# Kernel tuning notes

Hardware: AMD Instinct MI355X
Metric: run time of the kernel (lower is better)

Reference implementation:

```python
import jax, jax.numpy as jnp
import numpy as np

COEFF = 0.95

def _combine(c1, c2):
    # linear recurrence element: x_n = a_n * x_{n-1} + b_n
    a1, b1 = c1
    a2, b2 = c2
    return (a1 * a2, a2 * b1 + b2)

def setup_inputs() -> dict:
    key = jax.random.key(0)
    inputs = jax.random.normal(key, (64, 480000), dtype=jnp.float32)
    return {"inputs": inputs}

def reference(inputs) -> jnp.ndarray:
    # x[0] = e[0]; x[n] = COEFF * x[n-1] + e[n]
    # Expressed as parallel (Blelloch) scan over pairs (a, b) with a == COEFF.
    # a[0]'s value is irrelevant since the implicit x[-1] = 0.
    a = jnp.full_like(inputs, COEFF)
    _, x = jax.lax.associative_scan(_combine, (a, inputs), axis=1)
    return x
```

## Files before the change

### kernel.cpp

```cpp
#include <hip/hip_runtime.h>


#define ROW_N   480000
#define TILE    4096
#define WARM    512
#define NTILES  ((ROW_N + TILE - 1) / TILE)
#define NROWS   64

typedef float vfloat4 __attribute__((ext_vector_type(4)));

__global__ __launch_bounds__(1024)
void deemph_kernel(const float* __restrict__ in, float* __restrict__ out) {
    const int row      = blockIdx.y;
    const int startcol = blockIdx.x * TILE;
    const int tid      = threadIdx.x;
    const int lane     = tid & 63;
    const int wave     = tid >> 6;

    const float* __restrict__ rin  = in  + (size_t)row * ROW_N;
    float*       __restrict__ rout = out + (size_t)row * ROW_N;

    __shared__ float warr[16];
    __shared__ float wsum[16];

    const float LOG2C = -0.07400058144377693f;

    float wpart = 0.0f;
    if (startcol > 0 && tid < (WARM / 4)) {
        int wcol = startcol - WARM + tid * 4;
        vfloat4 v = *reinterpret_cast<const vfloat4*>(rin + wcol);
        float s = v.w;
        s = fmaf(0.95f,     v.z, s);
        s = fmaf(0.9025f,   v.y, s);
        s = fmaf(0.857375f, v.x, s);
        wpart = exp2f((float)(WARM - 4 - 4 * tid) * LOG2C) * s;
    }
    #pragma unroll
    for (int d = 1; d < 64; d <<= 1)
        wpart += __shfl_xor(wpart, d, 64);

    const int col    = startcol + tid * 4;
    const bool valid = (col < ROW_N);
    float e0 = 0.f, e1 = 0.f, e2 = 0.f, e3 = 0.f;
    if (valid) {
        vfloat4 v = *reinterpret_cast<const vfloat4*>(rin + col);
        e0 = v.x; e1 = v.y; e2 = v.z; e3 = v.w;
    }
    float l0 = e0;
    float l1 = fmaf(0.95f, l0, e1);
    float l2 = fmaf(0.95f, l1, e2);
    float l3 = fmaf(0.95f, l2, e3);

    const float M0 = 0.81450625f;
    const float M1 = 0.66342043f;
    const float M2 = 0.44012667f;
    const float M3 = 0.19371148f;
    const float M4 = 0.03752413f;
    const float M5 = 0.00140806f;
    float b = l3;
    { float t = __shfl_up(b, 1,  64); if (lane >= 1)  b = fmaf(M0, t, b); }
    { float t = __shfl_up(b, 2,  64); if (lane >= 2)  b = fmaf(M1, t, b); }
    { float t = __shfl_up(b, 4,  64); if (lane >= 4)  b = fmaf(M2, t, b); }
    { float t = __shfl_up(b, 8,  64); if (lane >= 8)  b = fmaf(M3, t, b); }
    { float t = __shfl_up(b, 16, 64); if (lane >= 16) b = fmaf(M4, t, b); }
    { float t = __shfl_up(b, 32, 64); if (lane >= 32) b = fmaf(M5, t, b); }

    float excl = __shfl_up(b, 1, 64);
    if (lane == 0) excl = 0.0f;

    if (lane == 63) warr[wave] = b;
    if (lane == 0)  wsum[wave] = wpart;
    __syncthreads();

    const float C256 = 1.9826347e-06f;
    float E = 0.0f;
    for (int u = 0; u < wave; ++u) E = fmaf(E, C256, warr[u]);
    float carry_warm = 0.0f;
    #pragma unroll
    for (int u = 0; u < 16; ++u) carry_warm += wsum[u];

    float pw = exp2f((float)(256 * wave) * LOG2C);
    float Sw = fmaf(pw, carry_warm, E);
    float pl = exp2f((float)(4 * lane) * LOG2C);
    float Q  = fmaf(pl, Sw, excl);

    if (valid) {
        vfloat4 r;
        r.x = fmaf(0.95f,       Q, l0);
        r.y = fmaf(0.9025f,     Q, l1);
        r.z = fmaf(0.857375f,   Q, l2);
        r.w = fmaf(0.81450625f, Q, l3);
        __builtin_nontemporal_store(r, reinterpret_cast<vfloat4*>(rout + col));
    }
}

extern "C" void kernel_launch(void* const* d_in, const int* in_sizes, int n_in,
                              void* d_out, int out_size, void* d_ws, size_t ws_size,
                              hipStream_t stream) {
    const float* in = (const float*)d_in[0];
    float* out = (float*)d_out;
    dim3 grid(NTILES, NROWS);
    deemph_kernel<<<grid, 1024, 0, stream>>>(in, out);
}
```

Measured before the change: 46.01 us.

## Process two half-tiles per block to halve warm-up overhead

Each block now covers an 8192-element tile as two 4096-element halves, with each thread handling one vec4 in each half. The high half's carry comes from the low half's wave totals instead of its own warm-up, so the 512-element warm-up read per tile is spread over twice as much data. All loads are issued up front so they overlap. In exchange there is more register pressure, the high half's carry chain is longer (serial over 16 wave totals), and only the high half has a bounds check: the low half relies on ROW_N not ending inside it.

```diff
diff --git a/kernel.cpp b/kernel.cpp
--- a/kernel.cpp
+++ b/kernel.cpp
@@ -2,7 +2,8 @@
 
 
 #define ROW_N   480000
-#define TILE    4096
+#define TILE    8192
+#define HALF    4096
 #define WARM    512
 #define NTILES  ((ROW_N + TILE - 1) / TILE)
 #define NROWS   64
@@ -20,36 +21,43 @@
     const float* __restrict__ rin  = in  + (size_t)row * ROW_N;
     float*       __restrict__ rout = out + (size_t)row * ROW_N;
 
-    __shared__ float warr[16];
+    __shared__ float warr[32];
     __shared__ float wsum[16];
 
     const float LOG2C = -0.07400058144377693f;
 
+    const int colL = startcol + tid * 4;
+    const int colH = startcol + HALF + tid * 4;
+    const bool vH  = (colH < ROW_N);
+
+    vfloat4 va = *reinterpret_cast<const vfloat4*>(rin + colL);
+    vfloat4 vb = {0.f, 0.f, 0.f, 0.f};
+    if (vH) vb = *reinterpret_cast<const vfloat4*>(rin + colH);
+    vfloat4 vw = {0.f, 0.f, 0.f, 0.f};
+    const bool doWarm = (startcol > 0) && (tid < (WARM / 4));
+    if (doWarm) vw = *reinterpret_cast<const vfloat4*>(rin + (startcol - WARM + tid * 4));
+
     float wpart = 0.0f;
-    if (startcol > 0 && tid < (WARM / 4)) {
-        int wcol = startcol - WARM + tid * 4;
-        vfloat4 v = *reinterpret_cast<const vfloat4*>(rin + wcol);
-        float s = v.w;
-        s = fmaf(0.95f,     v.z, s);
-        s = fmaf(0.9025f,   v.y, s);
-        s = fmaf(0.857375f, v.x, s);
+    if (doWarm) {
+        float s = vw.w;
+        s = fmaf(0.95f,     vw.z, s);
+        s = fmaf(0.9025f,   vw.y, s);
+        s = fmaf(0.857375f, vw.x, s);
         wpart = exp2f((float)(WARM - 4 - 4 * tid) * LOG2C) * s;
     }
     #pragma unroll
     for (int d = 1; d < 64; d <<= 1)
         wpart += __shfl_xor(wpart, d, 64);
+    if (lane == 0) wsum[wave] = wpart;
 
-    const int col    = startcol + tid * 4;
-    const bool valid = (col < ROW_N);
-    float e0 = 0.f, e1 = 0.f, e2 = 0.f, e3 = 0.f;
-    if (valid) {
-        vfloat4 v = *reinterpret_cast<const vfloat4*>(rin + col);
-        e0 = v.x; e1 = v.y; e2 = v.z; e3 = v.w;
-    }
-    float l0 = e0;
-    float l1 = fmaf(0.95f, l0, e1);
-    float l2 = fmaf(0.95f, l1, e2);
-    float l3 = fmaf(0.95f, l2, e3);
+    float l0 = va.x;
+    float l1 = fmaf(0.95f, l0, va.y);
+    float l2 = fmaf(0.95f, l1, va.z);
+    float l3 = fmaf(0.95f, l2, va.w);
+    float h0 = vb.x;
+    float h1 = fmaf(0.95f, h0, vb.y);
+    float h2 = fmaf(0.95f, h1, vb.z);
+    float h3 = fmaf(0.95f, h2, vb.w);
 
     const float M0 = 0.81450625f;
     const float M1 = 0.66342043f;
@@ -57,40 +65,52 @@
     const float M3 = 0.19371148f;
     const float M4 = 0.03752413f;
     const float M5 = 0.00140806f;
-    float b = l3;
-    { float t = __shfl_up(b, 1,  64); if (lane >= 1)  b = fmaf(M0, t, b); }
-    { float t = __shfl_up(b, 2,  64); if (lane >= 2)  b = fmaf(M1, t, b); }
-    { float t = __shfl_up(b, 4,  64); if (lane >= 4)  b = fmaf(M2, t, b); }
-    { float t = __shfl_up(b, 8,  64); if (lane >= 8)  b = fmaf(M3, t, b); }
-    { float t = __shfl_up(b, 16, 64); if (lane >= 16) b = fmaf(M4, t, b); }
-    { float t = __shfl_up(b, 32, 64); if (lane >= 32) b = fmaf(M5, t, b); }
+    float bL = l3, bH = h3;
+    { float t = __shfl_up(bL, 1,  64); float u = __shfl_up(bH, 1,  64); if (lane >= 1)  { bL = fmaf(M0, t, bL); bH = fmaf(M0, u, bH); } }
+    { float t = __shfl_up(bL, 2,  64); float u = __shfl_up(bH, 2,  64); if (lane >= 2)  { bL = fmaf(M1, t, bL); bH = fmaf(M1, u, bH); } }
+    { float t = __shfl_up(bL, 4,  64); float u = __shfl_up(bH, 4,  64); if (lane >= 4)  { bL = fmaf(M2, t, bL); bH = fmaf(M2, u, bH); } }
+    { float t = __shfl_up(bL, 8,  64); float u = __shfl_up(bH, 8,  64); if (lane >= 8)  { bL = fmaf(M3, t, bL); bH = fmaf(M3, u, bH); } }
+    { float t = __shfl_up(bL, 16, 64); float u = __shfl_up(bH, 16, 64); if (lane >= 16) { bL = fmaf(M4, t, bL); bH = fmaf(M4, u, bH); } }
+    { float t = __shfl_up(bL, 32, 64); float u = __shfl_up(bH, 32, 64); if (lane >= 32) { bL = fmaf(M5, t, bL); bH = fmaf(M5, u, bH); } }
 
-    float excl = __shfl_up(b, 1, 64);
-    if (lane == 0) excl = 0.0f;
+    float exL = __shfl_up(bL, 1, 64);
+    float exH = __shfl_up(bH, 1, 64);
+    if (lane == 0) { exL = 0.0f; exH = 0.0f; }
 
-    if (lane == 63) warr[wave] = b;
-    if (lane == 0)  wsum[wave] = wpart;
+    if (lane == 63) { warr[wave] = bL; warr[16 + wave] = bH; }
     __syncthreads();
 
     const float C256 = 1.9826347e-06f;
-    float E = 0.0f;
-    for (int u = 0; u < wave; ++u) E = fmaf(E, C256, warr[u]);
     float carry_warm = 0.0f;
     #pragma unroll
     for (int u = 0; u < 16; ++u) carry_warm += wsum[u];
 
+    float E = 0.0f;
+    for (int u = 0; u < wave; ++u) E = fmaf(E, C256, warr[u]);
+    float Eh = E;
+    for (int u = wave; u < 16 + wave; ++u) Eh = fmaf(Eh, C256, warr[u]);
+
     float pw = exp2f((float)(256 * wave) * LOG2C);
-    float Sw = fmaf(pw, carry_warm, E);
+    float SwL = fmaf(pw, carry_warm, E);
     float pl = exp2f((float)(4 * lane) * LOG2C);
-    float Q  = fmaf(pl, Sw, excl);
+    float QL = fmaf(pl, SwL, exL);
+    float QH = fmaf(pl, Eh,  exH);
 
-    if (valid) {
+    {
         vfloat4 r;
-        r.x = fmaf(0.95f,       Q, l0);
-        r.y = fmaf(0.9025f,     Q, l1);
-        r.z = fmaf(0.857375f,   Q, l2);
-        r.w = fmaf(0.81450625f, Q, l3);
-        __builtin_nontemporal_store(r, reinterpret_cast<vfloat4*>(rout + col));
+        r.x = fmaf(0.95f,       QL, l0);
+        r.y = fmaf(0.9025f,     QL, l1);
+        r.z = fmaf(0.857375f,   QL, l2);
+        r.w = fmaf(0.81450625f, QL, l3);
+        __builtin_nontemporal_store(r, reinterpret_cast<vfloat4*>(rout + colL));
+    }
+    if (vH) {
+        vfloat4 r;
+        r.x = fmaf(0.95f,       QH, h0);
+        r.y = fmaf(0.9025f,     QH, h1);
+        r.z = fmaf(0.857375f,   QH, h2);
+        r.w = fmaf(0.81450625f, QH, h3);
+        __builtin_nontemporal_store(r, reinterpret_cast<vfloat4*>(rout + colH));
     }
 }
 
```

Result: faster. 41.31 us (-10.2%).
